# Kernel optimization log

Measured on AMD Instinct MI355X. Metric: run time of the kernel, lower is better.

Reference implementation:

```python
import jax, jax.numpy as jnp
import numpy as np
from jax import lax

B, N, CIN, COUT, FPS, K, TCH, M, H = 8, 4096, 128, 256, 1024, 24, 256, 32, 4
HD = TCH // H
BN_SCALE = 1.0 / np.sqrt(1.0 + 1e-5)  # eval-mode BN: running_mean=0, running_var=1


def _gather(points, idx):
    # points [B,N,C], idx [B,S] or [B,S,K] -> gathered points
    return jax.vmap(lambda p, i: p[i])(points, idx)


def _bn(x, g, b):
    return x * (g * BN_SCALE) + b


def _ln(x, g, b):
    mu = jnp.mean(x, -1, keepdims=True)
    v = jnp.var(x, -1, keepdims=True)
    return (x - mu) / jnp.sqrt(v + 1e-5) * g + b


def _gelu(x):
    return jax.nn.gelu(x, approximate=False)


def _fps(xyz, npoint, farthest0):
    Bb, Nn, _ = xyz.shape
    def step(carry, _):
        dmin, far = carry
        c = jax.vmap(lambda p, i: p[i])(xyz, far)  # [B,3]
        d = jnp.sum((xyz - c[:, None, :]) ** 2, -1)
        dmin = jnp.minimum(dmin, d)
        return (dmin, jnp.argmax(dmin, -1)), far
    init = (jnp.full((Bb, Nn), 1e10, xyz.dtype), farthest0)
    _, cents = lax.scan(step, init, None, length=npoint)
    return cents.T  # [B, npoint]


def _sqdist(src, dst):
    d = -2.0 * jnp.einsum('bnc,bmc->bnm', src, dst)
    d = d + jnp.sum(src ** 2, -1)[:, :, None]
    d = d + jnp.sum(dst ** 2, -1)[:, None, :]
    return d


def _forward(xyz, x, t, farthest0, Wproj, gproj, bproj, Wl1, gl1, bl1, Wl2, gl2, bl2,
             Wc1, gc1, bc1, Wc2, gc2, bc2, Wq, Wk, Wv, Wo,
             ln1g, ln1b, Wqkv, Wao, ln2g, ln2b, Wf1, Wf2):
    # --- GenerateGraph: FPS + KNN grouping ---
    fps_idx = _fps(xyz, FPS, farthest0)            # [B,S]
    new_xyz = _gather(xyz, fps_idx)                # [B,S,3]
    xT = jnp.transpose(x, (0, 2, 1))               # [B,N,Cin]
    new_pts = _gather(xT, fps_idx)                 # [B,S,Cin]
    dist = _sqdist(new_xyz, xyz)                   # [B,S,N]
    _, idx = lax.top_k(-dist, K)                   # [B,S,K] nearest neighbors
    grouped = _gather(xT, idx)                     # [B,S,K,Cin]
    edge = grouped - new_pts[:, :, None, :]
    # --- Local: Conv1DBR proj + Conv1DBRRes (channels-last, 1x1 convs = GEMM) ---
    h = _gelu(_bn(jnp.einsum('bskc,oc->bsko', edge, Wproj), gproj, bproj))
    r = _gelu(_bn(jnp.einsum('bsko,po->bskp', h, Wl1), gl1, bl1))
    r = _bn(jnp.einsum('bskp,op->bsko', r, Wl2), gl2, bl2)
    h = _gelu(r + h)
    f = jnp.max(h, axis=2)                         # adaptive_max_pool over k -> [B,S,O]
    # --- Channel (ca): Conv1DBRRes on centroid features ---
    r = _gelu(_bn(f @ Wc1.T, gc1, bc1))
    r = _bn(r @ Wc2.T, gc2, bc2)
    f = _gelu(r + f)
    x_out = jnp.transpose(f, (0, 2, 1))            # [B,O,S]
    # --- Local2Former: tokens attend to local features ---
    q = t @ Wq.T
    kk = f @ Wk.T
    v = f @ Wv.T
    a = jax.nn.softmax(jnp.einsum('bmd,bsd->bms', q, kk) * (TCH ** -0.5), axis=-1)
    t = t + jnp.einsum('bms,bsd->bmd', a, v) @ Wo.T
    # --- Former: one pre-norm encoder layer (MHA + MLP) ---
    hn = _ln(t, ln1g, ln1b)
    qkv = (hn @ Wqkv.T).reshape(B, M, 3, H, HD).transpose(2, 0, 3, 1, 4)
    qh, kh, vh = qkv[0], qkv[1], qkv[2]            # [B,H,M,hd]
    attn = jax.nn.softmax(jnp.einsum('bhmd,bhnd->bhmn', qh, kh) * (HD ** -0.5), axis=-1)
    o = jnp.einsum('bhmn,bhnd->bhmd', attn, vh).transpose(0, 2, 1, 3).reshape(B, M, TCH)
    t = t + o @ Wao.T
    hn = _ln(t, ln2g, ln2b)
    t = t + _gelu(hn @ Wf1.T) @ Wf2.T
    return new_xyz, x_out, t


def setup_inputs() -> dict:
    key = jax.random.key(0)
    ks = jax.random.split(key, 40)
    def w(k, o, i):
        return jax.random.normal(k, (o, i), jnp.float32) / np.sqrt(i)
    def g(k, c):
        return 1.0 + 0.1 * jax.random.normal(k, (c,), jnp.float32)
    def bta(k, c):
        return 0.1 * jax.random.normal(k, (c,), jnp.float32)
    inp = {
        'xyz': jax.random.normal(ks[0], (B, N, 3), jnp.float32),
        'x': jax.random.normal(ks[1], (B, CIN, N), jnp.float32),
        't': jax.random.normal(ks[2], (B, M, TCH), jnp.float32),
        'farthest0': jax.random.randint(ks[3], (B,), 0, N),
        'Wproj': w(ks[4], COUT, CIN), 'gproj': g(ks[5], COUT), 'bproj': bta(ks[6], COUT),
        'Wl1': w(ks[7], COUT, COUT), 'gl1': g(ks[8], COUT), 'bl1': bta(ks[9], COUT),
        'Wl2': w(ks[10], COUT, COUT), 'gl2': g(ks[11], COUT), 'bl2': bta(ks[12], COUT),
        'Wc1': w(ks[13], COUT, COUT), 'gc1': g(ks[14], COUT), 'bc1': bta(ks[15], COUT),
        'Wc2': w(ks[16], COUT, COUT), 'gc2': g(ks[17], COUT), 'bc2': bta(ks[18], COUT),
        'Wq': w(ks[19], TCH, TCH), 'Wk': w(ks[20], TCH, COUT), 'Wv': w(ks[21], TCH, COUT),
        'Wo': w(ks[22], TCH, TCH),
        'ln1g': g(ks[23], TCH), 'ln1b': bta(ks[24], TCH),
        'Wqkv': w(ks[25], 3 * TCH, TCH), 'Wao': w(ks[26], TCH, TCH),
        'ln2g': g(ks[27], TCH), 'ln2b': bta(ks[28], TCH),
        'Wf1': w(ks[29], 2 * TCH, TCH), 'Wf2': w(ks[30], TCH, 2 * TCH),
    }
    return inp


def reference(xyz, x, t, farthest0, Wproj, gproj, bproj, Wl1, gl1, bl1, Wl2, gl2, bl2,
              Wc1, gc1, bc1, Wc2, gc2, bc2, Wq, Wk, Wv, Wo,
              ln1g, ln1b, Wqkv, Wao, ln2g, ln2b, Wf1, Wf2):
    return _forward(xyz, x, t, farthest0, Wproj, gproj, bproj, Wl1, gl1, bl1, Wl2, gl2, bl2,
                    Wc1, gc1, bc1, Wc2, gc2, bc2, Wq, Wk, Wv, Wo,
                    ln1g, ln1b, Wqkv, Wao, ln2g, ln2b, Wf1, Wf2)
```

## Files before the change

kernel.cpp:

```cpp
#include <hip/hip_runtime.h>
#include <math.h>

#define Bc 8
#define Nc 4096
#define CINc 128
#define COUTc 256
#define Sc 1024
#define Kc 24
#define TCHc 256
#define Mc 32
#define Hc 4
#define HDc 64
#define MBAT (Sc*Kc)

#define BN_SCALE_F 0.9999950000374997f

typedef __attribute__((ext_vector_type(8))) short bf16x8;
typedef __attribute__((ext_vector_type(4))) float f32x4;

__device__ __forceinline__ float b2f(short s){
  unsigned int u = ((unsigned int)(unsigned short)s) << 16;
  union { unsigned int u; float f; } c; c.u = u; return c.f;
}
__device__ __forceinline__ short f2b(float f){
  union { unsigned int u; float f; } c; c.f = f;
  unsigned int u = c.u;
  unsigned int r = (u + 0x7fffu + ((u >> 16) & 1u)) >> 16;
  return (short)(r & 0xffffu);
}
__device__ __forceinline__ float gelu_f(float v){
  return 0.5f * v * (1.f + erff(v * 0.7071067811865475f));
}
__device__ __forceinline__ float rdval(const float* p){ return *p; }
__device__ __forceinline__ float rdval(const short* p){ return b2f(*p); }
__device__ __forceinline__ void wrval(float* p, float v){ *p = v; }
__device__ __forceinline__ void wrval(short* p, float v){ *p = f2b(v); }

__device__ __forceinline__ void gl_lds16(const short* g, short* l){
  __builtin_amdgcn_global_load_lds(
     (const __attribute__((address_space(1))) void*)g,
     (__attribute__((address_space(3))) void*)l, 16, 0, 0);
}

__device__ __forceinline__ void bar_lds(){
  asm volatile("s_waitcnt lgkmcnt(0)" ::: "memory");
  __builtin_amdgcn_s_barrier();
}

template<int CTRL>
__device__ __forceinline__ double dpp_max_f64(double v){
  long long x = __double_as_longlong(v);
  int lo = (int)(unsigned int)(x & 0xFFFFFFFFLL);
  int hi = (int)(unsigned int)((unsigned long long)x >> 32);
  int plo = __builtin_amdgcn_update_dpp(lo, lo, CTRL, 0xF, 0xF, false);
  int phi = __builtin_amdgcn_update_dpp(hi, hi, CTRL, 0xF, 0xF, false);
  double p = __longlong_as_double((long long)(((unsigned long long)(unsigned int)phi << 32)
                                              | (unsigned int)plo));
  return fmax(v, p);
}
template<int CTRL>
__device__ __forceinline__ float dpp_min_f32(float v){
  int x = __float_as_int(v);
  int p = __builtin_amdgcn_update_dpp(x, x, CTRL, 0xF, 0xF, false);
  return fminf(v, __int_as_float(p));
}
template<int CTRL>
__device__ __forceinline__ unsigned dpp_min_u32(unsigned v){
  int p = __builtin_amdgcn_update_dpp((int)v, (int)v, CTRL, 0xF, 0xF, false);
  unsigned pu = (unsigned)p;
  return v < pu ? v : pu;
}

#define PREP_FPS 8
#define PREP_TOTAL 256
#define NWORK 248

__global__ __launch_bounds__(512) void prep_kernel(
    const float* __restrict__ xyz, const int* __restrict__ far0, int* __restrict__ fps_idx,
    const float* __restrict__ x, short* __restrict__ xT,
    const float* __restrict__ Wproj, const float* __restrict__ Wl1, const float* __restrict__ Wl2,
    const float* __restrict__ Wc1, const float* __restrict__ Wc2,
    const float* __restrict__ Wk, const float* __restrict__ Wv,
    const float* __restrict__ Wq, const float* __restrict__ Wo,
    const float* __restrict__ Wqkv, const float* __restrict__ Wao,
    const float* __restrict__ Wf1, const float* __restrict__ Wf2,
    const float* __restrict__ t_in,
    short* __restrict__ wbf,
    int* __restrict__ knn_idx, float* __restrict__ out0){
  __shared__ double smem[6176];
  int bid = blockIdx.x, tid = threadIdx.x;
  if(bid < PREP_FPS){
    int b = bid;
    float* sx = (float*)smem;
    float* sy = sx + Nc;
    float* sz = sy + Nc;
    double* pwave = smem + (Nc*12)/8;
    const float* xb = xyz + (size_t)b*Nc*3;
    for(int i=tid; i<Nc; i+=512){
      const float* p = xb + i*3;
      sx[i]=p[0]; sy[i]=p[1]; sz[i]=p[2];
    }
    __syncthreads();
    float px[8], py[8], pz[8], dmin[8];
    unsigned int lokey[8];
#pragma unroll
    for(int j=0;j<8;j++){
      int n = tid + 512*j;
      px[j]=sx[n]; py[j]=sy[n]; pz[j]=sz[n];
      dmin[j]=1e10f;
      lokey[j]=(unsigned int)((Nc-1) - n);
    }
    int winner = far0[b] & (Nc-1);
    int* out = fps_idx + b*Sc;
    for(int it=0; it<Sc; it++){
      if(tid==0)
        __hip_atomic_store(&out[it], winner, __ATOMIC_RELAXED, __HIP_MEMORY_SCOPE_AGENT);
      float cx=sx[winner], cy=sy[winner], cz=sz[winner];
      double key[8];
#pragma unroll
      for(int j=0;j<8;j++){
        float dx = __fsub_rn(px[j], cx);
        float dy = __fsub_rn(py[j], cy);
        float dz = __fsub_rn(pz[j], cz);
        float d = __fadd_rn(__fadd_rn(__fmul_rn(dx,dx), __fmul_rn(dy,dy)), __fmul_rn(dz,dz));
        dmin[j] = fminf(dmin[j], d);
        unsigned long long k = (((unsigned long long)__float_as_uint(dmin[j])) << 32) | lokey[j];
        key[j] = __longlong_as_double((long long)k);
      }
#pragma unroll
      for(int st=4; st>0; st>>=1)
#pragma unroll
        for(int j=0;j<st;j++) key[j] = fmax(key[j], key[j+st]);
      double kv = key[0];
      kv = dpp_max_f64<0x111>(kv);
      kv = dpp_max_f64<0x112>(kv);
      kv = dpp_max_f64<0x114>(kv);
      kv = dpp_max_f64<0x118>(kv);
      kv = dpp_max_f64<0x142>(kv);
      kv = dpp_max_f64<0x143>(kv);
      int p = it & 1;
      if((tid & 63) == 63) pwave[p*8 + (tid>>6)] = kv;
      bar_lds();
      double k0 = pwave[p*8+0], k1 = pwave[p*8+1], k2 = pwave[p*8+2], k3 = pwave[p*8+3];
      double k4 = pwave[p*8+4], k5 = pwave[p*8+5], k6 = pwave[p*8+6], k7 = pwave[p*8+7];
      double kb = fmax(fmax(fmax(k0,k1), fmax(k2,k3)), fmax(fmax(k4,k5), fmax(k6,k7)));
      unsigned long long kbits = (unsigned long long)__double_as_longlong(kb);
      winner = (Nc-1) - (int)(kbits & 0xFFFFFFFFULL);
    }
  } else {
    int wid = bid - PREP_FPS;
    int b = wid / 31;
    int widb = wid % 31;
    short (*tile)[33] = (short(*)[33])smem;
    for(int t = wid; t < 4096; t += NWORK){
      int bb = t >> 9;
      int rem = t & 511;
      int n0 = (rem & 127) * 32;
      int c0 = (rem >> 7) * 32;
      int tx = tid & 31, ty = tid >> 5;
      __syncthreads();
#pragma unroll
      for(int i=0;i<32;i+=16)
        tile[ty+i][tx] = f2b(x[((size_t)bb*CINc + (c0+ty+i))*Nc + n0+tx]);
      __syncthreads();
#pragma unroll
      for(int i=0;i<32;i+=16)
        xT[((size_t)bb*Nc + (n0+ty+i))*CINc + c0+tx] = tile[tx][ty+i];
    }
    {
      int gid = wid*512 + tid;
      const int stride = NWORK*512;
      short* p = wbf;
      for(int i=gid; i<COUTc*CINc; i+=stride) p[i] = f2b(Wproj[i]);
      p += COUTc*CINc;
      for(int i=gid; i<COUTc*COUTc; i+=stride) p[i] = f2b(Wl1[i]);
      p += COUTc*COUTc;
      for(int i=gid; i<COUTc*COUTc; i+=stride) p[i] = f2b(Wl2[i]);
      p += COUTc*COUTc;
      for(int i=gid; i<COUTc*COUTc; i+=stride) p[i] = f2b(Wc1[i]);
      p += COUTc*COUTc;
      for(int i=gid; i<COUTc*COUTc; i+=stride) p[i] = f2b(Wc2[i]);
      p += COUTc*COUTc;
      for(int i=gid; i<TCHc*COUTc; i+=stride) p[i] = f2b(Wk[i]);
      p += TCHc*COUTc;
      for(int i=gid; i<TCHc*COUTc; i+=stride) p[i] = f2b(Wv[i]);
      p += TCHc*COUTc;
      for(int i=gid; i<TCHc*TCHc; i+=stride) p[i] = f2b(Wq[i]);
      p += TCHc*TCHc;
      for(int i=gid; i<TCHc*TCHc; i+=stride) p[i] = f2b(Wo[i]);
      p += TCHc*TCHc;
      for(int i=gid; i<3*TCHc*TCHc; i+=stride) p[i] = f2b(Wqkv[i]);
      p += 3*TCHc*TCHc;
      for(int i=gid; i<TCHc*TCHc; i+=stride) p[i] = f2b(Wao[i]);
      p += TCHc*TCHc;
      for(int i=gid; i<2*TCHc*TCHc; i+=stride) p[i] = f2b(Wf1[i]);
      p += 2*TCHc*TCHc;
      for(int i=gid; i<2*TCHc*TCHc; i+=stride) p[i] = f2b(Wf2[i]);
      p += 2*TCHc*TCHc;
      for(int i=gid; i<Bc*Mc*TCHc; i+=stride) p[i] = f2b(t_in[i]);
    }
    int* s_qn = (int*)smem;
    float* pv = (float*)smem + 8;
    int*   pi = (int*)smem + 16;
    const float* xb = xyz + (size_t)b*Nc*3;
    float px[8], py[8], pz[8], db[8];
#pragma unroll
    for(int j=0;j<8;j++){
      int n = tid + 512*j;
      float xx=xb[n*3], yy=xb[n*3+1], zz=xb[n*3+2];
      px[j]=xx; py[j]=yy; pz[j]=zz;
      db[j] = __fadd_rn(__fadd_rn(__fmul_rn(xx,xx),__fmul_rn(yy,yy)),__fmul_rn(zz,zz));
    }
    __syncthreads();
    for(int s = widb; s < Sc; s += 31){
      if(tid==0){
        int qn;
        for(;;){
          qn = __hip_atomic_load(&fps_idx[b*Sc + s], __ATOMIC_RELAXED, __HIP_MEMORY_SCOPE_AGENT);
          if(qn >= 0) break;
          __builtin_amdgcn_s_sleep(8);
        }
        s_qn[0] = qn & (Nc-1);
      }
      bar_lds();
      int qn = s_qn[0];
      const float* q = xyz + ((size_t)b*Nc + qn)*3;
      float sxq = q[0], syq = q[1], szq = q[2];
      if(tid < 3) out0[((size_t)b*Sc + s)*3 + tid] = q[tid];
      float ss = __fadd_rn(__fadd_rn(__fmul_rn(sxq,sxq),__fmul_rn(syq,syq)),__fmul_rn(szq,szq));
      float dv[8];
#pragma unroll
      for(int j=0;j<8;j++){
        float e = __fmul_rn(sxq,px[j]);
        e = __fadd_rn(e, __fmul_rn(syq,py[j]));
        e = __fadd_rn(e, __fmul_rn(szq,pz[j]));
        dv[j] = __fadd_rn(__fadd_rn(__fmul_rn(-2.f,e), ss), db[j]);
      }
      int* ob = knn_idx + ((size_t)b*Sc + s)*Kc;
      for(int k=0;k<Kc;k++){
        float bvv = dv[0];
#pragma unroll
        for(int j=1;j<8;j++) bvv = fminf(bvv, dv[j]);
        bvv = dpp_min_f32<0x111>(bvv);
        bvv = dpp_min_f32<0x112>(bvv);
        bvv = dpp_min_f32<0x114>(bvv);
        bvv = dpp_min_f32<0x118>(bvv);
        bvv = dpp_min_f32<0x142>(bvv);
        bvv = dpp_min_f32<0x143>(bvv);
        if((tid&63)==63) pv[tid>>6] = bvv;
        bar_lds();
        float vmin = fminf(fminf(fminf(pv[0],pv[1]), fminf(pv[2],pv[3])),
                           fminf(fminf(pv[4],pv[5]), fminf(pv[6],pv[7])));
        unsigned bi = 0xFFFFFFFFu;
#pragma unroll
        for(int j=0;j<8;j++){
          unsigned n = (unsigned)(tid + 512*j);
          if(dv[j]==vmin && n < bi) bi = n;
        }
        bi = dpp_min_u32<0x111>(bi);
        bi = dpp_min_u32<0x112>(bi);
        bi = dpp_min_u32<0x114>(bi);
        bi = dpp_min_u32<0x118>(bi);
        bi = dpp_min_u32<0x142>(bi);
        bi = dpp_min_u32<0x143>(bi);
        if((tid&63)==63) pi[tid>>6] = (int)bi;
        bar_lds();
        unsigned win = (unsigned)pi[0];
#pragma unroll
        for(int w=1;w<8;w++){ unsigned u=(unsigned)pi[w]; win = u<win?u:win; }
        if(tid==0) ob[k] = (int)(win & (Nc-1));
#pragma unroll
        for(int j=0;j<8;j++) if((int)win == tid + 512*j) dv[j] = 3.4e38f;
      }
    }
  }
}

template<int HAS_BN, int HAS_GELU, int HAS_RES, typename TRES>
__global__ __launch_bounds__(256) void gemm128(
    const short* __restrict__ A, const short* __restrict__ W,
    const float* __restrict__ g, const float* __restrict__ bias,
    const TRES* __restrict__ Res, short* __restrict__ Out,
    int Nn, int Kk){
  __shared__ short As[128*32];
  __shared__ short Bs[128*32];
  int bm = blockIdx.y*128, bn = blockIdx.x*128;
  int tid = threadIdx.x;
  int wave = tid>>6, lane = tid&63, quad = lane>>4, l16 = lane&15;
  int wr = (wave>>1)*64, wc = (wave&1)*64;
  f32x4 acc[4][4];
#pragma unroll
  for(int i=0;i<4;i++)
#pragma unroll
    for(int j=0;j<4;j++) acc[i][j] = (f32x4){0.f,0.f,0.f,0.f};
  int sr = tid>>2, scc = (tid&3)*8;
  const short* Ap = A + (size_t)(bm+sr)*Kk + scc;
  const short* Wp = W + (size_t)(bn+sr)*Kk + scc;
  for(int k0=0; k0<Kk; k0+=32){
    gl_lds16(Ap + k0,                    As + tid*8);
    gl_lds16(Ap + k0 + (size_t)64*Kk,    As + 2048 + tid*8);
    gl_lds16(Wp + k0,                    Bs + tid*8);
    gl_lds16(Wp + k0 + (size_t)64*Kk,    Bs + 2048 + tid*8);
    __syncthreads();
    bf16x8 af[4], bfr[4];
#pragma unroll
    for(int mt=0; mt<4; mt++) af[mt]  = *(const bf16x8*)&As[(wr+mt*16+l16)*32 + quad*8];
#pragma unroll
    for(int nt=0; nt<4; nt++) bfr[nt] = *(const bf16x8*)&Bs[(wc+nt*16+l16)*32 + quad*8];
#pragma unroll
    for(int mt=0; mt<4; mt++)
#pragma unroll
      for(int nt=0; nt<4; nt++)
        acc[mt][nt] = __builtin_amdgcn_mfma_f32_16x16x32_bf16(af[mt], bfr[nt], acc[mt][nt], 0, 0, 0);
    __syncthreads();
  }
#pragma unroll
  for(int nt=0; nt<4; nt++){
    int col = bn + wc + nt*16 + l16;
    float gs = 0.f, bs_ = 0.f;
    if(HAS_BN){ gs = g[col] * BN_SCALE_F; bs_ = bias[col]; }
#pragma unroll
    for(int mt=0; mt<4; mt++){
#pragma unroll
      for(int r2=0;r2<4;r2++){
        int row = bm + wr + mt*16 + quad*4 + r2;
        float v = acc[mt][nt][r2];
        if(HAS_BN) v = v*gs + bs_;
        if(HAS_RES) v += rdval(Res + (size_t)row*Nn + col);
        if(HAS_GELU) v = gelu_f(v);
        Out[(size_t)row*Nn + col] = f2b(v);
      }
    }
  }
}

__global__ __launch_bounds__(256) void proj128(
    const short* __restrict__ xT, const int* __restrict__ knn_idx, const int* __restrict__ fps_idx,
    const short* __restrict__ W, const float* __restrict__ g, const float* __restrict__ bias,
    short* __restrict__ Out, int R0){
  __shared__ short As[128*32];
  __shared__ short Bs[128*32];
  int bm = blockIdx.y*128, bn = blockIdx.x*128;
  int tid = threadIdx.x;
  int wave = tid>>6, lane = tid&63, quad = lane>>4, l16 = lane&15;
  int wr = (wave>>1)*64, wc = (wave&1)*64;
  f32x4 acc[4][4];
#pragma unroll
  for(int i=0;i<4;i++)
#pragma unroll
    for(int j=0;j<4;j++) acc[i][j] = (f32x4){0.f,0.f,0.f,0.f};
  int sr = tid>>2, scc = (tid&3)*8;
  int Rg0 = R0 + bm + sr, Rg1 = Rg0 + 64;
  int b0 = Rg0 / (Sc*Kc), b1 = Rg1 / (Sc*Kc);
  int nk0 = knn_idx[Rg0] & (Nc-1), nk1 = knn_idx[Rg1] & (Nc-1);
  int nc0 = fps_idx[Rg0 / Kc] & (Nc-1), nc1 = fps_idx[Rg1 / Kc] & (Nc-1);
  const short* pk0 = xT + ((size_t)b0*Nc + nk0)*CINc + scc;
  const short* pc0 = xT + ((size_t)b0*Nc + nc0)*CINc + scc;
  const short* pk1 = xT + ((size_t)b1*Nc + nk1)*CINc + scc;
  const short* pc1 = xT + ((size_t)b1*Nc + nc1)*CINc + scc;
  const short* Wp  = W + (size_t)(bn+sr)*CINc + scc;
  for(int k0=0; k0<CINc; k0+=32){
    gl_lds16(Wp + k0,                      Bs + tid*8);
    gl_lds16(Wp + k0 + (size_t)64*CINc,    Bs + 2048 + tid*8);
    bf16x8 vk = *(const bf16x8*)(pk0 + k0);
    bf16x8 vc = *(const bf16x8*)(pc0 + k0);
    bf16x8 e0, e1;
#pragma unroll
    for(int i=0;i<8;i++) e0[i] = f2b(__fsub_rn(b2f(vk[i]), b2f(vc[i])));
    vk = *(const bf16x8*)(pk1 + k0);
    vc = *(const bf16x8*)(pc1 + k0);
#pragma unroll
    for(int i=0;i<8;i++) e1[i] = f2b(__fsub_rn(b2f(vk[i]), b2f(vc[i])));
    *(bf16x8*)&As[tid*8] = e0;
    *(bf16x8*)&As[2048 + tid*8] = e1;
    __syncthreads();
    bf16x8 af[4], bfr[4];
#pragma unroll
    for(int mt=0; mt<4; mt++) af[mt]  = *(const bf16x8*)&As[(wr+mt*16+l16)*32 + quad*8];
#pragma unroll
    for(int nt=0; nt<4; nt++) bfr[nt] = *(const bf16x8*)&Bs[(wc+nt*16+l16)*32 + quad*8];
#pragma unroll
    for(int mt=0; mt<4; mt++)
#pragma unroll
      for(int nt=0; nt<4; nt++)
        acc[mt][nt] = __builtin_amdgcn_mfma_f32_16x16x32_bf16(af[mt], bfr[nt], acc[mt][nt], 0, 0, 0);
    __syncthreads();
  }
#pragma unroll
  for(int nt=0; nt<4; nt++){
    int col = bn + wc + nt*16 + l16;
    float gs = g[col] * BN_SCALE_F, bs_ = bias[col];
#pragma unroll
    for(int mt=0; mt<4; mt++){
#pragma unroll
      for(int r2=0;r2<4;r2++){
        int row = bm + wr + mt*16 + quad*4 + r2;
        float v = acc[mt][nt][r2]*gs + bs_;
        Out[(size_t)row*COUTc + col] = f2b(gelu_f(v));
      }
    }
  }
}

__global__ __launch_bounds__(192) void gemm_l2max(
    const short* __restrict__ A, const short* __restrict__ W,
    const float* __restrict__ g, const float* __restrict__ bias,
    const short* __restrict__ Hres, short* __restrict__ Fout, int R0){
  __shared__ short As[48*32];
  __shared__ short Bs[64*32];
  __shared__ float sm[48][65];
  int bm = blockIdx.y*48, bn = blockIdx.x*64;
  int tid = threadIdx.x;
  int wave = tid >> 6, lane = tid & 63, quad = lane >> 4, l16 = lane & 15;
  f32x4 acc[4];
#pragma unroll
  for(int i=0;i<4;i++) acc[i] = (f32x4){0.f,0.f,0.f,0.f};
  const short* Ap  = A + (size_t)(bm + (tid>>2))*COUTc + (tid&3)*8;
  const short* Wp  = W + (size_t)(bn + (tid>>2))*COUTc + (tid&3)*8;
  const short* Wp2 = W + (size_t)(bn + 48 + (lane>>2))*COUTc + (lane&3)*8;
  for(int k0=0; k0<COUTc; k0+=32){
    gl_lds16(Ap + k0, As + tid*8);
    gl_lds16(Wp + k0, Bs + tid*8);
    if(wave==0) gl_lds16(Wp2 + k0, Bs + 1536 + lane*8);
    __syncthreads();
    bf16x8 a = *(const bf16x8*)&As[(wave*16 + l16)*32 + quad*8];
// ... 298 lines not shown
```

Before: 1.141 ms.

## Spatially bin points per wave in FPS and skip waves beyond the current max distance

Sorts each batch's points into 64 spatial cells (a 4x4x4 grid ordered Morton-style) so that each wave owns a compact region, and computes a per-wave bounding box. On each FPS iteration a wave skips its distance update when the new centroid's distance to its box is at least the wave's current max min-distance, and reuses its previous key instead. This removes distance work for far regions but adds a sort with LDS atomics and a larger shared-memory footprint. The grid bounds assume coordinates lie roughly in [-4.2, 4.2], and the skip test uses a 1.0001 slack factor.

```diff
diff --git a/kernel.cpp b/kernel.cpp
--- a/kernel.cpp
+++ b/kernel.cpp
@@ -65,10 +65,29 @@
   return fminf(v, __int_as_float(p));
 }
 template<int CTRL>
+__device__ __forceinline__ float dpp_max_f32(float v){
+  int x = __float_as_int(v);
+  int p = __builtin_amdgcn_update_dpp(x, x, CTRL, 0xF, 0xF, false);
+  return fmaxf(v, __int_as_float(p));
+}
+template<int CTRL>
 __device__ __forceinline__ unsigned dpp_min_u32(unsigned v){
   int p = __builtin_amdgcn_update_dpp((int)v, (int)v, CTRL, 0xF, 0xF, false);
   unsigned pu = (unsigned)p;
   return v < pu ? v : pu;
+}
+__device__ __forceinline__ float wave_min63(float v){
+  v = dpp_min_f32<0x111>(v); v = dpp_min_f32<0x112>(v); v = dpp_min_f32<0x114>(v);
+  v = dpp_min_f32<0x118>(v); v = dpp_min_f32<0x142>(v); v = dpp_min_f32<0x143>(v);
+  return v;
+}
+__device__ __forceinline__ float wave_max63(float v){
+  v = dpp_max_f32<0x111>(v); v = dpp_max_f32<0x112>(v); v = dpp_max_f32<0x114>(v);
+  v = dpp_max_f32<0x118>(v); v = dpp_max_f32<0x142>(v); v = dpp_max_f32<0x143>(v);
+  return v;
+}
+__device__ __forceinline__ float bcast63(float v){
+  return __int_as_float(__builtin_amdgcn_readlane(__float_as_int(v), 63));
 }
 
 #define PREP_FPS 8
@@ -87,59 +106,106 @@
     const float* __restrict__ t_in,
     short* __restrict__ wbf,
     int* __restrict__ knn_idx, float* __restrict__ out0){
-  __shared__ double smem[6176];
+  __shared__ __align__(16) char smemc[57728];
   int bid = blockIdx.x, tid = threadIdx.x;
   if(bid < PREP_FPS){
     int b = bid;
-    float* sx = (float*)smem;
-    float* sy = sx + Nc;
-    float* sz = sy + Nc;
-    double* pwave = smem + (Nc*12)/8;
+    float* sxyz = (float*)smemc;
+    unsigned short* sid = (unsigned short*)(smemc + 49152);
+    int* hist = (int*)(smemc + 57344);
+    double* pwave = (double*)(smemc + 57600);
     const float* xb = xyz + (size_t)b*Nc*3;
+    if(tid < 64) hist[tid] = 0;
+    float gx[8], gy[8], gz[8]; int code[8];
+    __syncthreads();
+#pragma unroll
+    for(int j=0;j<8;j++){
+      int n = tid + 512*j;
+      const float* p = xb + n*3;
+      gx[j]=p[0]; gy[j]=p[1]; gz[j]=p[2];
+      int qx = (int)fminf(fmaxf((gx[j]+4.2f)*(4.f/8.4f),0.f),3.f);
+      int qy = (int)fminf(fmaxf((gy[j]+4.2f)*(4.f/8.4f),0.f),3.f);
+      int qz = (int)fminf(fmaxf((gz[j]+4.2f)*(4.f/8.4f),0.f),3.f);
+      code[j] = ((qx>>1)<<5)|((qy>>1)<<4)|((qz>>1)<<3)|((qx&1)<<2)|((qy&1)<<1)|(qz&1);
+      atomicAdd(&hist[code[j]], 1);
+    }
+    __syncthreads();
+    if(tid==0){
+      int run=0;
+      for(int i=0;i<64;i++){ int h=hist[i]; hist[i]=run; run+=h; }
+    }
+    __syncthreads();
+#pragma unroll
+    for(int j=0;j<8;j++){
+      int slot = atomicAdd(&hist[code[j]], 1);
+      sxyz[slot*3]=gx[j]; sxyz[slot*3+1]=gy[j]; sxyz[slot*3+2]=gz[j];
+      sid[slot] = (unsigned short)(tid + 512*j);
+    }
+    __syncthreads();
+    float px[8], py[8], pz[8], dmin[8];
+    unsigned int lokey[8];
+    float mnx=3e38f,mny=3e38f,mnz=3e38f,mxx=-3e38f,mxy=-3e38f,mxz=-3e38f;
+#pragma unroll
+    for(int j=0;j<8;j++){
+      int i = (tid>>6)*512 + j*64 + (tid&63);
+      float xx=sxyz[i*3], yy=sxyz[i*3+1], zz=sxyz[i*3+2];
+      px[j]=xx; py[j]=yy; pz[j]=zz;
+      dmin[j]=1e10f;
+      lokey[j]=(unsigned int)((Nc-1) - (int)sid[i]);
+      mnx=fminf(mnx,xx); mxx=fmaxf(mxx,xx);
+      mny=fminf(mny,yy); mxy=fmaxf(mxy,yy);
+      mnz=fminf(mnz,zz); mxz=fmaxf(mxz,zz);
+    }
+    float bbmnx = bcast63(wave_min63(mnx)), bbmxx = bcast63(wave_max63(mxx));
+    float bbmny = bcast63(wave_min63(mny)), bbmxy = bcast63(wave_max63(mxy));
+    float bbmnz = bcast63(wave_min63(mnz)), bbmxz = bcast63(wave_max63(mxz));
+    __syncthreads();
     for(int i=tid; i<Nc; i+=512){
       const float* p = xb + i*3;
-      sx[i]=p[0]; sy[i]=p[1]; sz[i]=p[2];
-    }
-    __syncthreads();
-    float px[8], py[8], pz[8], dmin[8];
-    unsigned int lokey[8];
-#pragma unroll
-    for(int j=0;j<8;j++){
-      int n = tid + 512*j;
-      px[j]=sx[n]; py[j]=sy[n]; pz[j]=sz[n];
-      dmin[j]=1e10f;
-      lokey[j]=(unsigned int)((Nc-1) - n);
-    }
+      sxyz[i*3]=p[0]; sxyz[i*3+1]=p[1]; sxyz[i*3+2]=p[2];
+    }
+    __syncthreads();
     int winner = far0[b] & (Nc-1);
     int* out = fps_idx + b*Sc;
+    double pk = 0.0;
+    float wm = 3.0e38f;
     for(int it=0; it<Sc; it++){
       if(tid==0)
         __hip_atomic_store(&out[it], winner, __ATOMIC_RELAXED, __HIP_MEMORY_SCOPE_AGENT);
-      float cx=sx[winner], cy=sy[winner], cz=sz[winner];
-      double key[8];
-#pragma unroll
-      for(int j=0;j<8;j++){
-        float dx = __fsub_rn(px[j], cx);
-        float dy = __fsub_rn(py[j], cy);
-        float dz = __fsub_rn(pz[j], cz);
-        float d = __fadd_rn(__fadd_rn(__fmul_rn(dx,dx), __fmul_rn(dy,dy)), __fmul_rn(dz,dz));
-        dmin[j] = fminf(dmin[j], d);
-        unsigned long long k = (((unsigned long long)__float_as_uint(dmin[j])) << 32) | lokey[j];
-        key[j] = __longlong_as_double((long long)k);
+      float cx=sxyz[winner*3], cy=sxyz[winner*3+1], cz=sxyz[winner*3+2];
+      float ddx = fmaxf(fmaxf(bbmnx - cx, cx - bbmxx), 0.f);
+      float ddy = fmaxf(fmaxf(bbmny - cy, cy - bbmxy), 0.f);
+      float ddz = fmaxf(fmaxf(bbmnz - cz, cz - bbmxz), 0.f);
+      float md2 = ddx*ddx + ddy*ddy + ddz*ddz;
+      if(md2 < wm*1.0001f){
+        double key[8];
+#pragma unroll
+        for(int j=0;j<8;j++){
+          float dx = __fsub_rn(px[j], cx);
+          float dy = __fsub_rn(py[j], cy);
+          float dz = __fsub_rn(pz[j], cz);
+          float d = __fadd_rn(__fadd_rn(__fmul_rn(dx,dx), __fmul_rn(dy,dy)), __fmul_rn(dz,dz));
+          dmin[j] = fminf(dmin[j], d);
+          unsigned long long k = (((unsigned long long)__float_as_uint(dmin[j])) << 32) | lokey[j];
+          key[j] = __longlong_as_double((long long)k);
+        }
+#pragma unroll
+        for(int st=4; st>0; st>>=1)
+#pragma unroll
+          for(int j=0;j<st;j++) key[j] = fmax(key[j], key[j+st]);
+        double kv = key[0];
+        kv = dpp_max_f64<0x111>(kv);
+        kv = dpp_max_f64<0x112>(kv);
+        kv = dpp_max_f64<0x114>(kv);
+        kv = dpp_max_f64<0x118>(kv);
+        kv = dpp_max_f64<0x142>(kv);
+        kv = dpp_max_f64<0x143>(kv);
+        pk = kv;
+        wm = __int_as_float(__builtin_amdgcn_readlane(
+               (int)(__double_as_longlong(kv) >> 32), 63));
       }
-#pragma unroll
-      for(int st=4; st>0; st>>=1)
-#pragma unroll
-        for(int j=0;j<st;j++) key[j] = fmax(key[j], key[j+st]);
-      double kv = key[0];
-      kv = dpp_max_f64<0x111>(kv);
-      kv = dpp_max_f64<0x112>(kv);
-      kv = dpp_max_f64<0x114>(kv);
-      kv = dpp_max_f64<0x118>(kv);
-      kv = dpp_max_f64<0x142>(kv);
-      kv = dpp_max_f64<0x143>(kv);
       int p = it & 1;
-      if((tid & 63) == 63) pwave[p*8 + (tid>>6)] = kv;
+      if((tid & 63) == 63) pwave[p*8 + (tid>>6)] = pk;
       bar_lds();
       double k0 = pwave[p*8+0], k1 = pwave[p*8+1], k2 = pwave[p*8+2], k3 = pwave[p*8+3];
       double k4 = pwave[p*8+4], k5 = pwave[p*8+5], k6 = pwave[p*8+6], k7 = pwave[p*8+7];
@@ -151,7 +217,7 @@
     int wid = bid - PREP_FPS;
     int b = wid / 31;
     int widb = wid % 31;
-    short (*tile)[33] = (short(*)[33])smem;
+    short (*tile)[33] = (short(*)[33])smemc;
     for(int t = wid; t < 4096; t += NWORK){
       int bb = t >> 9;
       int rem = t & 511;
@@ -199,9 +265,9 @@
       p += 2*TCHc*TCHc;
       for(int i=gid; i<Bc*Mc*TCHc; i+=stride) p[i] = f2b(t_in[i]);
     }
-    int* s_qn = (int*)smem;
-    float* pv = (float*)smem + 8;
-    int*   pi = (int*)smem + 16;
+    int* s_qn = (int*)smemc;
+    float* pv = (float*)(smemc + 32);
+    int*   pi = (int*)(smemc + 64);
     const float* xb = xyz + (size_t)b*Nc*3;
     float px[8], py[8], pz[8], db[8];
 #pragma unroll
```

Result: no change. 1.132 ms (-0.8%).

## Speculate FPS winners from per-wave top-2 candidates and fuse KNN argmin keys

Applied to the files above, without the earlier changes.

FPS now reduces a top-2 key, together with the winner's coordinates, per wave. It keeps the 8 per-wave leaders as candidates so that later iterations can be resolved without a block barrier while the best candidate stays above every runner-up bound. The point coordinates also travel with the reduction, which removes the LDS staging of xyz. KNN selection packs distance and index into one 64-bit key, so each of the K steps needs one reduction and one barrier instead of two. The speculative FPS path carries extra register state and depends on exact tie-breaking. The KNN change clamps negative distances to zero, which could change ordering on ties.

```diff
diff --git a/kernel.cpp b/kernel.cpp
--- a/kernel.cpp
+++ b/kernel.cpp
@@ -47,28 +47,50 @@
   __builtin_amdgcn_s_barrier();
 }
 
+__device__ __forceinline__ double packkey(float d, unsigned tag){
+  return __longlong_as_double((long long)(
+    (((unsigned long long)(unsigned)__float_as_int(d)) << 32) | (unsigned long long)tag));
+}
+__device__ __forceinline__ double pack2f(float a, float b){
+  return __longlong_as_double((long long)(
+    (((unsigned long long)(unsigned)__float_as_int(b)) << 32) | (unsigned)__float_as_int(a)));
+}
+
 template<int CTRL>
-__device__ __forceinline__ double dpp_max_f64(double v){
+__device__ __forceinline__ double dpp_mov_f64(double v){
   long long x = __double_as_longlong(v);
-  int lo = (int)(unsigned int)(x & 0xFFFFFFFFLL);
-  int hi = (int)(unsigned int)((unsigned long long)x >> 32);
+  int lo = (int)(unsigned)(x & 0xFFFFFFFFLL);
+  int hi = (int)(unsigned)((unsigned long long)x >> 32);
   int plo = __builtin_amdgcn_update_dpp(lo, lo, CTRL, 0xF, 0xF, false);
   int phi = __builtin_amdgcn_update_dpp(hi, hi, CTRL, 0xF, 0xF, false);
-  double p = __longlong_as_double((long long)(((unsigned long long)(unsigned int)phi << 32)
-                                              | (unsigned int)plo));
-  return fmax(v, p);
+  return __longlong_as_double((long long)(((unsigned long long)(unsigned)phi << 32)
+                                          | (unsigned)plo));
 }
 template<int CTRL>
-__device__ __forceinline__ float dpp_min_f32(float v){
-  int x = __float_as_int(v);
-  int p = __builtin_amdgcn_update_dpp(x, x, CTRL, 0xF, 0xF, false);
-  return fminf(v, __int_as_float(p));
+__device__ __forceinline__ float dpp_mov_f32(float v){
+  int p = __builtin_amdgcn_update_dpp(__float_as_int(v), __float_as_int(v), CTRL, 0xF, 0xF, false);
+  return __int_as_float(p);
 }
 template<int CTRL>
-__device__ __forceinline__ unsigned dpp_min_u32(unsigned v){
-  int p = __builtin_amdgcn_update_dpp((int)v, (int)v, CTRL, 0xF, 0xF, false);
-  unsigned pu = (unsigned)p;
-  return v < pu ? v : pu;
+__device__ __forceinline__ double dpp_min_f64(double v){
+  return fmin(v, dpp_mov_f64<CTRL>(v));
+}
+template<int CTRL>
+__device__ __forceinline__ void top2_step(double& k1, double& k2, float& x, float& y, float& z){
+  double p1 = dpp_mov_f64<CTRL>(k1);
+  double p2 = dpp_mov_f64<CTRL>(k2);
+  float qx = dpp_mov_f32<CTRL>(x);
+  float qy = dpp_mov_f32<CTRL>(y);
+  float qz = dpp_mov_f32<CTRL>(z);
+  double n1 = fmax(k1, p1);
+  double lo = fmin(k1, p1);
+  double c1 = (lo == n1) ? 0.0 : lo;
+  double c2 = (k2 == n1) ? 0.0 : k2;
+  double c3 = (p2 == n1) ? 0.0 : p2;
+  double n2 = fmax(c1, fmax(c2, c3));
+  bool s = p1 > k1;
+  x = s ? qx : x; y = s ? qy : y; z = s ? qz : z;
+  k1 = n1; k2 = n2;
 }
 
 #define PREP_FPS 8
@@ -87,36 +109,31 @@
     const float* __restrict__ t_in,
     short* __restrict__ wbf,
     int* __restrict__ knn_idx, float* __restrict__ out0){
-  __shared__ double smem[6176];
+  __shared__ __align__(16) char smemc[57728];
   int bid = blockIdx.x, tid = threadIdx.x;
   if(bid < PREP_FPS){
     int b = bid;
-    float* sx = (float*)smem;
-    float* sy = sx + Nc;
-    float* sz = sy + Nc;
-    double* pwave = smem + (Nc*12)/8;
+    double* pwave = (double*)smemc;
     const float* xb = xyz + (size_t)b*Nc*3;
-    for(int i=tid; i<Nc; i+=512){
-      const float* p = xb + i*3;
-      sx[i]=p[0]; sy[i]=p[1]; sz[i]=p[2];
-    }
-    __syncthreads();
     float px[8], py[8], pz[8], dmin[8];
-    unsigned int lokey[8];
 #pragma unroll
     for(int j=0;j<8;j++){
       int n = tid + 512*j;
-      px[j]=sx[n]; py[j]=sy[n]; pz[j]=sz[n];
+      const float* p = xb + n*3;
+      px[j]=p[0]; py[j]=p[1]; pz[j]=p[2];
       dmin[j]=1e10f;
-      lokey[j]=(unsigned int)((Nc-1) - n);
-    }
-    int winner = far0[b] & (Nc-1);
+    }
     int* out = fps_idx + b*Sc;
-    for(int it=0; it<Sc; it++){
-      if(tid==0)
-        __hip_atomic_store(&out[it], winner, __ATOMIC_RELAXED, __HIP_MEMORY_SCOPE_AGENT);
-      float cx=sx[winner], cy=sy[winner], cz=sz[winner];
-      double key[8];
+    int far0idx = far0[b] & (Nc-1);
+    float cx = xb[far0idx*3], cy = xb[far0idx*3+1], cz = xb[far0idx*3+2];
+    if(tid==0)
+      __hip_atomic_store(&out[0], far0idx, __ATOMIC_RELAXED, __HIP_MEMORY_SCOPE_AGENT);
+    double cand_key[8]; unsigned cand_lo[8]; float cdx[8], cdy[8], cdz[8];
+#pragma unroll
+    for(int i=0;i<8;i++){ cand_key[i]=0.0; cand_lo[i]=0u; cdx[i]=0.f; cdy[i]=0.f; cdz[i]=0.f; }
+    double B = 1e300;
+    int it = 1, fr = 0;
+    while(true){
 #pragma unroll
       for(int j=0;j<8;j++){
         float dx = __fsub_rn(px[j], cx);
@@ -124,34 +141,97 @@
         float dz = __fsub_rn(pz[j], cz);
         float d = __fadd_rn(__fadd_rn(__fmul_rn(dx,dx), __fmul_rn(dy,dy)), __fmul_rn(dz,dz));
         dmin[j] = fminf(dmin[j], d);
-        unsigned long long k = (((unsigned long long)__float_as_uint(dmin[j])) << 32) | lokey[j];
-        key[j] = __longlong_as_double((long long)k);
-      }
-#pragma unroll
-      for(int st=4; st>0; st>>=1)
-#pragma unroll
-        for(int j=0;j<st;j++) key[j] = fmax(key[j], key[j+st]);
-      double kv = key[0];
-      kv = dpp_max_f64<0x111>(kv);
-      kv = dpp_max_f64<0x112>(kv);
-      kv = dpp_max_f64<0x114>(kv);
-      kv = dpp_max_f64<0x118>(kv);
-      kv = dpp_max_f64<0x142>(kv);
-      kv = dpp_max_f64<0x143>(kv);
-      int p = it & 1;
-      if((tid & 63) == 63) pwave[p*8 + (tid>>6)] = kv;
+      }
+#pragma unroll
+      for(int i=0;i<8;i++){
+        float dx = __fsub_rn(cdx[i], cx);
+        float dy = __fsub_rn(cdy[i], cy);
+        float dz = __fsub_rn(cdz[i], cz);
+        float d = __fadd_rn(__fadd_rn(__fmul_rn(dx,dx), __fmul_rn(dy,dy)), __fmul_rn(dz,dz));
+        cand_key[i] = fmin(cand_key[i], packkey(d, cand_lo[i]));
+      }
+      double m = cand_key[0]; int slot = 0;
+      float wx = cdx[0], wy = cdy[0], wz = cdz[0];
+#pragma unroll
+      for(int i=1;i<8;i++){
+        bool s = cand_key[i] > m;
+        m = s ? cand_key[i] : m; slot = s ? i : slot;
+        wx = s ? cdx[i] : wx; wy = s ? cdy[i] : wy; wz = s ? cdz[i] : wz;
+      }
+      if(m >= B){
+        int idx = (Nc-1) - (int)(unsigned)(__double_as_longlong(m) & 0xFFFFFFFFULL);
+        if(tid==0)
+          __hip_atomic_store(&out[it], idx, __ATOMIC_RELAXED, __HIP_MEMORY_SCOPE_AGENT);
+        cx = wx; cy = wy; cz = wz;
+#pragma unroll
+        for(int i=0;i<8;i++) if(i==slot) cand_key[i] = 0.0;
+        if(++it == Sc) break;
+        continue;
+      }
+      double m1, m2; float X, Y, Z;
+      {
+        m1 = packkey(dmin[0], (unsigned)((Nc-1) - tid));
+        m2 = 0.0; X = px[0]; Y = py[0]; Z = pz[0];
+#pragma unroll
+        for(int j=1;j<8;j++){
+          double kj = packkey(dmin[j], (unsigned)((Nc-1) - (tid + 512*j)));
+          double lo = fmin(m1, kj);
+          m2 = fmax(m2, lo);
+          bool s = kj > m1;
+          X = s ? px[j] : X; Y = s ? py[j] : Y; Z = s ? pz[j] : Z;
+          m1 = fmax(m1, kj);
+        }
+      }
+      top2_step<0x111>(m1,m2,X,Y,Z);
+      top2_step<0x112>(m1,m2,X,Y,Z);
+      top2_step<0x114>(m1,m2,X,Y,Z);
+      top2_step<0x118>(m1,m2,X,Y,Z);
+      top2_step<0x142>(m1,m2,X,Y,Z);
+      top2_step<0x143>(m1,m2,X,Y,Z);
+      double* row = pwave + (fr&1)*32 + (tid>>6)*4;
+      if((tid&63)==63){
+        row[0]=m1; row[1]=m2; row[2]=pack2f(X,Y); row[3]=pack2f(Z,0.f);
+      }
       bar_lds();
-      double k0 = pwave[p*8+0], k1 = pwave[p*8+1], k2 = pwave[p*8+2], k3 = pwave[p*8+3];
-      double k4 = pwave[p*8+4], k5 = pwave[p*8+5], k6 = pwave[p*8+6], k7 = pwave[p*8+7];
-      double kb = fmax(fmax(fmax(k0,k1), fmax(k2,k3)), fmax(fmax(k4,k5), fmax(k6,k7)));
-      unsigned long long kbits = (unsigned long long)__double_as_longlong(kb);
-      winner = (Nc-1) - (int)(kbits & 0xFFFFFFFFULL);
+      const double* basep = pwave + (fr&1)*32;
+      fr++;
+      double K[8]; float XX[8], YY[8], ZZ[8]; double Bn = 0.0;
+#pragma unroll
+      for(int i=0;i<8;i++){
+        K[i] = basep[i*4+0];
+        Bn = fmax(Bn, basep[i*4+1]);
+        long long bxy = __double_as_longlong(basep[i*4+2]);
+        XX[i] = __int_as_float((int)(unsigned)(bxy & 0xFFFFFFFFLL));
+        YY[i] = __int_as_float((int)(unsigned)((unsigned long long)bxy >> 32));
+        ZZ[i] = __int_as_float((int)(unsigned)(__double_as_longlong(basep[i*4+3]) & 0xFFFFFFFFLL));
+      }
+      double mm = K[0]; int sl = 0; float wx2 = XX[0], wy2 = YY[0], wz2 = ZZ[0];
+#pragma unroll
+      for(int i=1;i<8;i++){
+        bool s = K[i] > mm;
+        mm = s ? K[i] : mm; sl = s ? i : sl;
+        wx2 = s ? XX[i] : wx2; wy2 = s ? YY[i] : wy2; wz2 = s ? ZZ[i] : wz2;
+      }
+      B = Bn;
+#pragma unroll
+      for(int i=0;i<8;i++){
+        cand_key[i] = K[i];
+        cand_lo[i] = (unsigned)(__double_as_longlong(K[i]) & 0xFFFFFFFFULL);
+        cdx[i] = XX[i]; cdy[i] = YY[i]; cdz[i] = ZZ[i];
+      }
+#pragma unroll
+      for(int i=0;i<8;i++) if(i==sl) cand_key[i] = 0.0;
+      int idx = (Nc-1) - (int)(unsigned)(__double_as_longlong(mm) & 0xFFFFFFFFULL);
+      if(tid==0)
+        __hip_atomic_store(&out[it], idx, __ATOMIC_RELAXED, __HIP_MEMORY_SCOPE_AGENT);
+      cx = wx2; cy = wy2; cz = wz2;
+      if(++it == Sc) break;
     }
   } else {
     int wid = bid - PREP_FPS;
     int b = wid / 31;
     int widb = wid % 31;
-    short (*tile)[33] = (short(*)[33])smem;
+    short (*tile)[33] = (short(*)[33])smemc;
     for(int t = wid; t < 4096; t += NWORK){
       int bb = t >> 9;
       int rem = t & 511;
@@ -199,9 +279,8 @@
       p += 2*TCHc*TCHc;
       for(int i=gid; i<Bc*Mc*TCHc; i+=stride) p[i] = f2b(t_in[i]);
     }
-    int* s_qn = (int*)smem;
-    float* pv = (float*)smem + 8;
-    int*   pi = (int*)smem + 16;
+    int* s_qn = (int*)(smemc + 2112);
+    double* pvd = (double*)(smemc + 2176);
     const float* xb = xyz + (size_t)b*Nc*3;
     float px[8], py[8], pz[8], db[8];
 #pragma unroll
@@ -238,39 +317,24 @@
       }
       int* ob = knn_idx + ((size_t)b*Sc + s)*Kc;
       for(int k=0;k<Kc;k++){
-        float bvv = dv[0];
-#pragma unroll
-        for(int j=1;j<8;j++) bvv = fminf(bvv, dv[j]);
-        bvv = dpp_min_f32<0x111>(bvv);
-        bvv = dpp_min_f32<0x112>(bvv);
-        bvv = dpp_min_f32<0x114>(bvv);
-        bvv = dpp_min_f32<0x118>(bvv);
-        bvv = dpp_min_f32<0x142>(bvv);
-        bvv = dpp_min_f32<0x143>(bvv);
-        if((tid&63)==63) pv[tid>>6] = bvv;
+        double kk = packkey(fmaxf(dv[0],0.f), (unsigned)tid);
+#pragma unroll
+        for(int j=1;j<8;j++) kk = fmin(kk, packkey(fmaxf(dv[j],0.f), (unsigned)(tid + 512*j)));
+        kk = dpp_min_f64<0x111>(kk);
+        kk = dpp_min_f64<0x112>(kk);
+        kk = dpp_min_f64<0x114>(kk);
+        kk = dpp_min_f64<0x118>(kk);
+        kk = dpp_min_f64<0x142>(kk);
+        kk = dpp_min_f64<0x143>(kk);
+        double* pb = pvd + (k&1)*8;
+        if((tid&63)==63) pb[tid>>6] = kk;
         bar_lds();
-        float vmin = fminf(fminf(fminf(pv[0],pv[1]), fminf(pv[2],pv[3])),
-                           fminf(fminf(pv[4],pv[5]), fminf(pv[6],pv[7])));
-        unsigned bi = 0xFFFFFFFFu;
-#pragma unroll
-        for(int j=0;j<8;j++){
-          unsigned n = (unsigned)(tid + 512*j);
-          if(dv[j]==vmin && n < bi) bi = n;
-        }
-        bi = dpp_min_u32<0x111>(bi);
-        bi = dpp_min_u32<0x112>(bi);
-        bi = dpp_min_u32<0x114>(bi);
-        bi = dpp_min_u32<0x118>(bi);
-        bi = dpp_min_u32<0x142>(bi);
-        bi = dpp_min_u32<0x143>(bi);
-        if((tid&63)==63) pi[tid>>6] = (int)bi;
-        bar_lds();
-        unsigned win = (unsigned)pi[0];
-#pragma unroll
-        for(int w=1;w<8;w++){ unsigned u=(unsigned)pi[w]; win = u<win?u:win; }
-        if(tid==0) ob[k] = (int)(win & (Nc-1));
-#pragma unroll
-        for(int j=0;j<8;j++) if((int)win == tid + 512*j) dv[j] = 3.4e38f;
+        double w0 = fmin(fmin(fmin(pb[0],pb[1]),fmin(pb[2],pb[3])),
+                         fmin(fmin(pb[4],pb[5]),fmin(pb[6],pb[7])));
+        int win = (int)(unsigned)(__double_as_longlong(w0) & 0xFFFFFFFFULL);
+        if(tid==0) ob[k] = win;
+#pragma unroll
+        for(int j=0;j<8;j++) if(tid + 512*j == win) dv[j] = 3.4e38f;
       }
     }
   }
```

Result: slower. 1.627 ms (+42.5%).

## Streamline FPS and KNN argmax reductions with packed math and single-barrier keys

Applied to the files above, without the earlier changes.

The FPS loop now assigns each thread 8 contiguous points and computes distances with packed v_pk_add/v_pk_mul. It reduces only a float max across the wave with DPP, then recovers the argmax index via ballot and readlane, instead of doing a 64-bit key reduction. The KNN top-k loop packs distance and index into one double key, so each of the 24 selections needs a single DPP min reduction and one barrier instead of two passes and two barriers. This shortens the serial per-iteration latency of the FPS critical path and the KNN selection. It relies on positive-float bit ordering through the double comparison, clamping negative distances to zero, and ballot-based tie-breaking to keep the same first-index semantics.

```diff
diff --git a/kernel.cpp b/kernel.cpp
--- a/kernel.cpp
+++ b/kernel.cpp
@@ -17,6 +17,7 @@
 
 typedef __attribute__((ext_vector_type(8))) short bf16x8;
 typedef __attribute__((ext_vector_type(4))) float f32x4;
+typedef __attribute__((ext_vector_type(2))) float f32x2;
 
 __device__ __forceinline__ float b2f(short s){
   unsigned int u = ((unsigned int)(unsigned short)s) << 16;
@@ -47,28 +48,36 @@
   __builtin_amdgcn_s_barrier();
 }
 
+__device__ __forceinline__ f32x2 pk_add(f32x2 a, f32x2 b){
+  f32x2 d; asm("v_pk_add_f32 %0, %1, %2" : "=v"(d) : "v"(a), "v"(b)); return d;
+}
+__device__ __forceinline__ f32x2 pk_mul(f32x2 a, f32x2 b){
+  f32x2 d; asm("v_pk_mul_f32 %0, %1, %2" : "=v"(d) : "v"(a), "v"(b)); return d;
+}
+
+__device__ __forceinline__ double packkey(float d, unsigned tag){
+  return __longlong_as_double((long long)(
+    (((unsigned long long)(unsigned)__float_as_int(d)) << 32) | (unsigned long long)tag));
+}
+
 template<int CTRL>
-__device__ __forceinline__ double dpp_max_f64(double v){
+__device__ __forceinline__ double dpp_mov_f64(double v){
   long long x = __double_as_longlong(v);
-  int lo = (int)(unsigned int)(x & 0xFFFFFFFFLL);
-  int hi = (int)(unsigned int)((unsigned long long)x >> 32);
+  int lo = (int)(unsigned)(x & 0xFFFFFFFFLL);
+  int hi = (int)(unsigned)((unsigned long long)x >> 32);
   int plo = __builtin_amdgcn_update_dpp(lo, lo, CTRL, 0xF, 0xF, false);
   int phi = __builtin_amdgcn_update_dpp(hi, hi, CTRL, 0xF, 0xF, false);
-  double p = __longlong_as_double((long long)(((unsigned long long)(unsigned int)phi << 32)
-                                              | (unsigned int)plo));
-  return fmax(v, p);
+  return __longlong_as_double((long long)(((unsigned long long)(unsigned)phi << 32)
+                                          | (unsigned)plo));
 }
 template<int CTRL>
-__device__ __forceinline__ float dpp_min_f32(float v){
-  int x = __float_as_int(v);
-  int p = __builtin_amdgcn_update_dpp(x, x, CTRL, 0xF, 0xF, false);
-  return fminf(v, __int_as_float(p));
+__device__ __forceinline__ double dpp_min_f64(double v){
+  return fmin(v, dpp_mov_f64<CTRL>(v));
 }
 template<int CTRL>
-__device__ __forceinline__ unsigned dpp_min_u32(unsigned v){
-  int p = __builtin_amdgcn_update_dpp((int)v, (int)v, CTRL, 0xF, 0xF, false);
-  unsigned pu = (unsigned)p;
-  return v < pu ? v : pu;
+__device__ __forceinline__ float dpp_max_f32(float v){
+  int p = __builtin_amdgcn_update_dpp(__float_as_int(v), __float_as_int(v), CTRL, 0xF, 0xF, false);
+  return fmaxf(v, __int_as_float(p));
 }
 
 #define PREP_FPS 8
@@ -87,28 +96,30 @@
     const float* __restrict__ t_in,
     short* __restrict__ wbf,
     int* __restrict__ knn_idx, float* __restrict__ out0){
-  __shared__ double smem[6176];
+  __shared__ __align__(16) char smemc[57728];
   int bid = blockIdx.x, tid = threadIdx.x;
   if(bid < PREP_FPS){
     int b = bid;
-    float* sx = (float*)smem;
+    float* sx = (float*)smemc;
     float* sy = sx + Nc;
     float* sz = sy + Nc;
-    double* pwave = smem + (Nc*12)/8;
+    double* pwave = (double*)(smemc + 49152);
     const float* xb = xyz + (size_t)b*Nc*3;
     for(int i=tid; i<Nc; i+=512){
       const float* p = xb + i*3;
       sx[i]=p[0]; sy[i]=p[1]; sz[i]=p[2];
     }
     __syncthreads();
-    float px[8], py[8], pz[8], dmin[8];
-    unsigned int lokey[8];
-#pragma unroll
-    for(int j=0;j<8;j++){
-      int n = tid + 512*j;
-      px[j]=sx[n]; py[j]=sy[n]; pz[j]=sz[n];
-      dmin[j]=1e10f;
-      lokey[j]=(unsigned int)((Nc-1) - n);
+    int lane = tid & 63, wv = tid >> 6;
+    int base = wv*512 + lane*8;
+    f32x2 px2[4], py2[4], pz2[4];
+    float dmn[8];
+#pragma unroll
+    for(int i=0;i<4;i++){
+      px2[i] = (f32x2){ sx[base+2*i], sx[base+2*i+1] };
+      py2[i] = (f32x2){ sy[base+2*i], sy[base+2*i+1] };
+      pz2[i] = (f32x2){ sz[base+2*i], sz[base+2*i+1] };
+      dmn[2*i] = 1e10f; dmn[2*i+1] = 1e10f;
     }
     int winner = far0[b] & (Nc-1);
     int* out = fps_idx + b*Sc;
@@ -116,42 +127,46 @@
       if(tid==0)
         __hip_atomic_store(&out[it], winner, __ATOMIC_RELAXED, __HIP_MEMORY_SCOPE_AGENT);
       float cx=sx[winner], cy=sy[winner], cz=sz[winner];
-      double key[8];
-#pragma unroll
-      for(int j=0;j<8;j++){
-        float dx = __fsub_rn(px[j], cx);
-        float dy = __fsub_rn(py[j], cy);
-        float dz = __fsub_rn(pz[j], cz);
-        float d = __fadd_rn(__fadd_rn(__fmul_rn(dx,dx), __fmul_rn(dy,dy)), __fmul_rn(dz,dz));
-        dmin[j] = fminf(dmin[j], d);
-        unsigned long long k = (((unsigned long long)__float_as_uint(dmin[j])) << 32) | lokey[j];
-        key[j] = __longlong_as_double((long long)k);
+      f32x2 ncx = (f32x2){-cx,-cx}, ncy = (f32x2){-cy,-cy}, ncz = (f32x2){-cz,-cz};
+      float vmax = -1.f;
+#pragma unroll
+      for(int i=0;i<4;i++){
+        f32x2 dx = pk_add(px2[i], ncx);
+        f32x2 dy = pk_add(py2[i], ncy);
+        f32x2 dz = pk_add(pz2[i], ncz);
+        f32x2 d  = pk_add(pk_add(pk_mul(dx,dx), pk_mul(dy,dy)), pk_mul(dz,dz));
+        dmn[2*i]   = fminf(dmn[2*i],   d[0]);
+        dmn[2*i+1] = fminf(dmn[2*i+1], d[1]);
+        vmax = fmaxf(vmax, fmaxf(dmn[2*i], dmn[2*i+1]));
       }
-#pragma unroll
-      for(int st=4; st>0; st>>=1)
-#pragma unroll
-        for(int j=0;j<st;j++) key[j] = fmax(key[j], key[j+st]);
-      double kv = key[0];
-      kv = dpp_max_f64<0x111>(kv);
-      kv = dpp_max_f64<0x112>(kv);
-      kv = dpp_max_f64<0x114>(kv);
-      kv = dpp_max_f64<0x118>(kv);
-      kv = dpp_max_f64<0x142>(kv);
-      kv = dpp_max_f64<0x143>(kv);
-      int p = it & 1;
-      if((tid & 63) == 63) pwave[p*8 + (tid>>6)] = kv;
+      float wm = vmax;
+      wm = dpp_max_f32<0x111>(wm);
+      wm = dpp_max_f32<0x112>(wm);
+      wm = dpp_max_f32<0x114>(wm);
+      wm = dpp_max_f32<0x118>(wm);
+      wm = dpp_max_f32<0x142>(wm);
+      wm = dpp_max_f32<0x143>(wm);
+      float smax = __int_as_float(__builtin_amdgcn_readlane(__float_as_int(wm), 63));
+      int lj = 0;
+#pragma unroll
+      for(int j=7;j>=0;j--) if(dmn[j]==smax) lj = j;
+      unsigned long long mk = __ballot(vmax == smax);
+      int flane = __ffsll(mk) - 1;
+      int ljw = __builtin_amdgcn_readlane(lj, flane);
+      int widx = wv*512 + flane*8 + ljw;
+      if(lane==0)
+        pwave[(it&1)*8 + wv] = packkey(smax, (unsigned)((Nc-1) - widx));
       bar_lds();
-      double k0 = pwave[p*8+0], k1 = pwave[p*8+1], k2 = pwave[p*8+2], k3 = pwave[p*8+3];
-      double k4 = pwave[p*8+4], k5 = pwave[p*8+5], k6 = pwave[p*8+6], k7 = pwave[p*8+7];
-      double kb = fmax(fmax(fmax(k0,k1), fmax(k2,k3)), fmax(fmax(k4,k5), fmax(k6,k7)));
-      unsigned long long kbits = (unsigned long long)__double_as_longlong(kb);
-      winner = (Nc-1) - (int)(kbits & 0xFFFFFFFFULL);
+      const double* pb = pwave + (it&1)*8;
+      double kb = fmax(fmax(fmax(pb[0],pb[1]), fmax(pb[2],pb[3])),
+                       fmax(fmax(pb[4],pb[5]), fmax(pb[6],pb[7])));
+      winner = (Nc-1) - (int)(unsigned)(__double_as_longlong(kb) & 0xFFFFFFFFULL);
     }
   } else {
     int wid = bid - PREP_FPS;
     int b = wid / 31;
     int widb = wid % 31;
-    short (*tile)[33] = (short(*)[33])smem;
+    short (*tile)[33] = (short(*)[33])smemc;
     for(int t = wid; t < 4096; t += NWORK){
       int bb = t >> 9;
       int rem = t & 511;
@@ -199,9 +214,8 @@
       p += 2*TCHc*TCHc;
       for(int i=gid; i<Bc*Mc*TCHc; i+=stride) p[i] = f2b(t_in[i]);
     }
-    int* s_qn = (int*)smem;
-    float* pv = (float*)smem + 8;
-    int*   pi = (int*)smem + 16;
+    int* s_qn = (int*)(smemc + 2112);
+    double* pvd = (double*)(smemc + 2176);
     const float* xb = xyz + (size_t)b*Nc*3;
     float px[8], py[8], pz[8], db[8];
 #pragma unroll
@@ -238,39 +252,24 @@
       }
       int* ob = knn_idx + ((size_t)b*Sc + s)*Kc;
       for(int k=0;k<Kc;k++){
-        float bvv = dv[0];
-#pragma unroll
-        for(int j=1;j<8;j++) bvv = fminf(bvv, dv[j]);
-        bvv = dpp_min_f32<0x111>(bvv);
-        bvv = dpp_min_f32<0x112>(bvv);
-        bvv = dpp_min_f32<0x114>(bvv);
-        bvv = dpp_min_f32<0x118>(bvv);
-        bvv = dpp_min_f32<0x142>(bvv);
-        bvv = dpp_min_f32<0x143>(bvv);
-        if((tid&63)==63) pv[tid>>6] = bvv;
+        double kk = packkey(fmaxf(dv[0],0.f), (unsigned)tid);
+#pragma unroll
+        for(int j=1;j<8;j++) kk = fmin(kk, packkey(fmaxf(dv[j],0.f), (unsigned)(tid + 512*j)));
+        kk = dpp_min_f64<0x111>(kk);
+        kk = dpp_min_f64<0x112>(kk);
+        kk = dpp_min_f64<0x114>(kk);
+        kk = dpp_min_f64<0x118>(kk);
+        kk = dpp_min_f64<0x142>(kk);
+        kk = dpp_min_f64<0x143>(kk);
+        double* pb = pvd + (k&1)*8;
+        if((tid&63)==63) pb[tid>>6] = kk;
         bar_lds();
-        float vmin = fminf(fminf(fminf(pv[0],pv[1]), fminf(pv[2],pv[3])),
-                           fminf(fminf(pv[4],pv[5]), fminf(pv[6],pv[7])));
-        unsigned bi = 0xFFFFFFFFu;
-#pragma unroll
-        for(int j=0;j<8;j++){
-          unsigned n = (unsigned)(tid + 512*j);
-          if(dv[j]==vmin && n < bi) bi = n;
-        }
-        bi = dpp_min_u32<0x111>(bi);
-        bi = dpp_min_u32<0x112>(bi);
-        bi = dpp_min_u32<0x114>(bi);
-        bi = dpp_min_u32<0x118>(bi);
-        bi = dpp_min_u32<0x142>(bi);
-        bi = dpp_min_u32<0x143>(bi);
-        if((tid&63)==63) pi[tid>>6] = (int)bi;
-        bar_lds();
-        unsigned win = (unsigned)pi[0];
-#pragma unroll
-        for(int w=1;w<8;w++){ unsigned u=(unsigned)pi[w]; win = u<win?u:win; }
-        if(tid==0) ob[k] = (int)(win & (Nc-1));
-#pragma unroll
-        for(int j=0;j<8;j++) if((int)win == tid + 512*j) dv[j] = 3.4e38f;
+        double w0 = fmin(fmin(fmin(pb[0],pb[1]),fmin(pb[2],pb[3])),
+                         fmin(fmin(pb[4],pb[5]),fmin(pb[6],pb[7])));
+        int win = (int)(unsigned)(__double_as_longlong(w0) & 0xFFFFFFFFULL);
+        if(tid==0) ob[k] = win;
+#pragma unroll
+        for(int j=0;j<8;j++) if(tid + 512*j == win) dv[j] = 3.4e38f;
       }
     }
   }
```

After: 1.257 ms. 1.1x slower.
